# Optimization experiments

Measured on AMD Instinct MI355X. Metric: run time of the kernel, lower is better.

Reference implementation:

```python
import jax, jax.numpy as jnp
import numpy as np

N_NODES = 50000
N_EDGES = 800000
D = 128  # d_feat == hidden_channels


def setup_inputs() -> dict:
    key = jax.random.key(0)
    ks = jax.random.split(key, 7)
    s = 1.0 / np.sqrt(D)
    return {
        "x": jax.random.normal(ks[0], (N_NODES, D), dtype=jnp.float32),
        "edge_index": jax.random.randint(ks[1], (2, N_EDGES), 0, N_NODES, dtype=jnp.int64),
        "W1_l": jax.random.normal(ks[2], (D, D), dtype=jnp.float32) * s,
        "b1": jnp.zeros((D,), dtype=jnp.float32),
        "W1_r": jax.random.normal(ks[3], (D, D), dtype=jnp.float32) * s,
        "W2_l": jax.random.normal(ks[4], (D, D), dtype=jnp.float32) * s,
        "b2": jnp.zeros((D,), dtype=jnp.float32),
        "W2_r": jax.random.normal(ks[5], (D, D), dtype=jnp.float32) * s,
    }


def reference(x, edge_index, W1_l, b1, W1_r, W2_l, b2, W2_r):
    src = edge_index[0]
    dst = edge_index[1]
    n = x.shape[0]
    # in-degree for mean aggregation (zero-degree nodes get 0 aggregate)
    deg = jax.ops.segment_sum(jnp.ones_like(src, dtype=x.dtype), dst, num_segments=n)
    inv_deg = (1.0 / jnp.maximum(deg, 1.0))[:, None]  # [N,1]

    def sage_conv(h, Wl, b, Wr):
        # mean over incoming neighbor messages, then lin_l(agg) + lin_r(h)
        agg = jax.ops.segment_sum(h[src], dst, num_segments=n) * inv_deg  # [N,D]
        return agg @ Wl + b + h @ Wr

    h = jax.nn.relu(sage_conv(x, W1_l, b1, W1_r))
    return sage_conv(h, W2_l, b2, W2_r)
```

## Files before the change

### kernel.cpp

```cpp
#include <hip/hip_runtime.h>
#include <hip/hip_bf16.h>

typedef __attribute__((ext_vector_type(8))) short bf16x8;
typedef __attribute__((ext_vector_type(4))) float f32x4;

#define CAP 64
#define SH  8

static __device__ inline unsigned short f2b(float f) {
    unsigned u = __float_as_uint(f);
    unsigned r = (u + 0x7FFFu + ((u >> 16) & 1u)) >> 16;
    return (unsigned short)r;
}
static __device__ inline float blo(unsigned u) { return __uint_as_float(u << 16); }
static __device__ inline float bhi(unsigned u) { return __uint_as_float(u & 0xFFFF0000u); }

__global__ void zero_kernel(int* __restrict__ p, int n) {
    int i = blockIdx.x * blockDim.x + threadIdx.x;
    if (i < n) p[i] = 0;
}

__global__ __launch_bounds__(256) void fill_shard_kernel(
        const int* __restrict__ ei, int* __restrict__ cursor,
        unsigned short* __restrict__ edge16, int E, int N, int G, int npg) {
    int s = blockIdx.x & (SH - 1);
    int i = blockIdx.x >> 3;
    int d_lo = s * npg;
    int d_hi = d_lo + npg; if (d_hi > N) d_hi = N;
    int C = (E + G - 1) / G;
    int e0 = i * C;
    int e1 = e0 + C; if (e1 > E) e1 = E;
    for (int e = e0 + threadIdx.x; e < e1; e += 256) {
        int d = ei[E + e];
        if (d < d_lo || d >= d_hi) continue;
        int src = ei[e];
        if ((unsigned)src >= (unsigned)N) src = 0;
        int pos = atomicAdd(&cursor[d], 1);
        if (pos < CAP) edge16[(size_t)d * CAP + pos] = (unsigned short)src;
    }
}

__global__ __launch_bounds__(256) void x2b_kernel(const float* __restrict__ x,
                                                  unsigned short* __restrict__ xb,
                                                  int n4) {
    int i = blockIdx.x * blockDim.x + threadIdx.x;
    if (i >= n4) return;
    float4 v = ((const float4*)x)[i];
    ushort4 b;
    b.x = f2b(v.x); b.y = f2b(v.y); b.z = f2b(v.z); b.w = f2b(v.w);
    ((ushort4*)xb)[i] = b;
}

__global__ void prep_w_kernel(const float* __restrict__ W1l, const float* __restrict__ W1r,
                              const float* __restrict__ W2l, const float* __restrict__ W2r,
                              unsigned short* __restrict__ wt) {
    int n = blockIdx.x & 127;
    int layer = blockIdx.x >> 7;
    int k = threadIdx.x;
    const float* Wlp = layer ? W2l : W1l;
    const float* Wrp = layer ? W2r : W1r;
    unsigned short* dst = wt + (size_t)layer * 128 * 256 + (size_t)n * 256;
    dst[k]       = f2b(Wlp[(size_t)k * 128 + n]);
    dst[k + 128] = f2b(Wrp[(size_t)k * 128 + n]);
}

template<int RELU, int OUT_BF16>
__global__ __launch_bounds__(256) void layer_kernel(
        const unsigned short* __restrict__ in, const int* __restrict__ cursor,
        const unsigned short* __restrict__ edge16, const int* __restrict__ ei,
        const unsigned short* __restrict__ Wt, const float* __restrict__ bias,
        void* __restrict__ outp, int E, int N) {
    constexpr int LDK = 264;
    __shared__ unsigned short sA[64 * LDK];
    int tid  = threadIdx.x;
    int lane = tid & 63;
    int wave = tid >> 6;
    int row0 = blockIdx.x * 64;

    #pragma unroll
    for (int it = 0; it < 4; ++it) {
        int c = tid + it * 256;
        int r = c >> 4;
        int q = c & 15;
        int row = row0 + r; if (row >= N) row = N - 1;
        uint4 v = ((const uint4*)(in + (size_t)row * 128))[q];
        *(uint4*)&sA[r * LDK + 128 + q * 8] = v;
    }

    int g = lane >> 4;
    int f = lane & 15;
    for (int i = 0; i < 16; ++i) {
        int node = row0 + wave * 16 + i;
        if (node >= N) break;
        int deg = cursor[node];
        float acc[8];
        #pragma unroll
        for (int t = 0; t < 8; ++t) acc[t] = 0.f;

        if (deg <= CAP) {
            const unsigned short* base = edge16 + (size_t)node * CAP;
            int idx = (lane < deg) ? (int)base[lane] : 0;
            #pragma unroll 4
            for (int j = 0; j < deg; j += 4) {
                int e = j + g;
                int s = __shfl(idx, e & 63);
                if (e < deg) {
                    uint4 v = *(const uint4*)(in + (size_t)s * 128 + f * 8);
                    acc[0] += blo(v.x); acc[1] += bhi(v.x);
                    acc[2] += blo(v.y); acc[3] += bhi(v.y);
                    acc[4] += blo(v.z); acc[5] += bhi(v.z);
                    acc[6] += blo(v.w); acc[7] += bhi(v.w);
                }
            }
        } else {
            for (int j = 0; j < E; j += 4) {
                int e = j + g;
                bool act = (e < E) && (ei[E + e] == node);
                if (act) {
                    int s = ei[e];
                    if ((unsigned)s >= (unsigned)N) s = 0;
                    uint4 v = *(const uint4*)(in + (size_t)s * 128 + f * 8);
                    acc[0] += blo(v.x); acc[1] += bhi(v.x);
                    acc[2] += blo(v.y); acc[3] += bhi(v.y);
                    acc[4] += blo(v.z); acc[5] += bhi(v.z);
                    acc[6] += blo(v.w); acc[7] += bhi(v.w);
                }
            }
        }
        #pragma unroll
        for (int d = 16; d <= 32; d <<= 1) {
            #pragma unroll
            for (int t = 0; t < 8; ++t) acc[t] += __shfl_xor(acc[t], d);
        }
        if (g == 0) {
            float inv = 1.0f / (float)(deg > 1 ? deg : 1);
            uint4 o;
            o.x = (unsigned)f2b(acc[0] * inv) | ((unsigned)f2b(acc[1] * inv) << 16);
            o.y = (unsigned)f2b(acc[2] * inv) | ((unsigned)f2b(acc[3] * inv) << 16);
            o.z = (unsigned)f2b(acc[4] * inv) | ((unsigned)f2b(acc[5] * inv) << 16);
            o.w = (unsigned)f2b(acc[6] * inv) | ((unsigned)f2b(acc[7] * inv) << 16);
            *(uint4*)&sA[(wave * 16 + i) * LDK + f * 8] = o;
        }
    }
    __syncthreads();

    int quad = lane >> 4;
    int tm   = lane & 15;

    f32x4 acc[4][2];
    #pragma unroll
    for (int m = 0; m < 4; ++m)
        #pragma unroll
        for (int j = 0; j < 2; ++j)
            acc[m][j] = (f32x4){0.f, 0.f, 0.f, 0.f};

    const unsigned short* wb0 = Wt + (size_t)(wave * 32 + tm) * 256;

    #pragma unroll
    for (int ks = 0; ks < 8; ++ks) {
        int k0 = ks * 32 + quad * 8;
        bf16x8 a[4], b[2];
        #pragma unroll
        for (int m = 0; m < 4; ++m)
            a[m] = *(const bf16x8*)&sA[(m * 16 + tm) * LDK + k0];
        #pragma unroll
        for (int j = 0; j < 2; ++j)
            b[j] = *(const bf16x8*)(wb0 + (size_t)j * 16 * 256 + k0);
        #pragma unroll
        for (int m = 0; m < 4; ++m)
            #pragma unroll
            for (int j = 0; j < 2; ++j)
                acc[m][j] = __builtin_amdgcn_mfma_f32_16x16x32_bf16(a[m], b[j], acc[m][j], 0, 0, 0);
    }

    #pragma unroll
    for (int j = 0; j < 2; ++j) {
        int ncol = wave * 32 + j * 16 + tm;
        float bb = bias[ncol];
        #pragma unroll
        for (int m = 0; m < 4; ++m) {
            #pragma unroll
            for (int reg = 0; reg < 4; ++reg) {
                int row = row0 + m * 16 + quad * 4 + reg;
                if (row >= N) continue;
                float v = acc[m][j][reg] + bb;
                if (RELU) v = v > 0.f ? v : 0.f;
                if (OUT_BF16)
                    ((unsigned short*)outp)[(size_t)row * 128 + ncol] = f2b(v);
                else
                    ((float*)outp)[(size_t)row * 128 + ncol] = v;
            }
        }
    }
}

extern "C" void kernel_launch(void* const* d_in, const int* in_sizes, int n_in,
                              void* d_out, int out_size, void* d_ws, size_t ws_size,
                              hipStream_t stream) {
    const float* x   = (const float*)d_in[0];
    const int*   ei  = (const int*)d_in[1];
    const float* W1l = (const float*)d_in[2];
    const float* b1  = (const float*)d_in[3];
    const float* W1r = (const float*)d_in[4];
    const float* W2l = (const float*)d_in[5];
    const float* b2  = (const float*)d_in[6];
    const float* W2r = (const float*)d_in[7];
    float* out = (float*)d_out;

    const int D = 128;
    const int N = in_sizes[0] / D;
    const int E = in_sizes[1] / 2;

    char* ws = (char*)d_ws;
    size_t off = 0;
    auto alloc = [&](size_t bytes) {
        size_t o = off;
        off = (off + bytes + 511) & ~(size_t)511;
        return (void*)(ws + o);
    };
    int*            cursor  = (int*)           alloc((size_t)N * 4);
    unsigned short* edge16  = (unsigned short*)alloc((size_t)N * CAP * 2);
    unsigned short* xb      = (unsigned short*)alloc((size_t)N * D * 2);
    unsigned short* h_bf    = (unsigned short*)alloc((size_t)N * D * 2);
    unsigned short* wt      = (unsigned short*)alloc((size_t)2 * 128 * 256 * 2);
    (void)ws_size; (void)n_in; (void)out_size;

    zero_kernel<<<(N + 255) / 256, 256, 0, stream>>>(cursor, N);
    {
        int G = 256;
        int npg = (N + SH - 1) / SH;
        fill_shard_kernel<<<SH * G, 256, 0, stream>>>(ei, cursor, edge16, E, N, G, npg);
    }

    int n4 = N * D / 4;
    x2b_kernel<<<(n4 + 255) / 256, 256, 0, stream>>>(x, xb, n4);
    prep_w_kernel<<<256, 128, 0, stream>>>(W1l, W1r, W2l, W2r, wt);
    const unsigned short* wt1 = wt;
    const unsigned short* wt2 = wt + (size_t)128 * 256;

    int grid = (N + 63) / 64;

    layer_kernel<1, 1><<<grid, 256, 0, stream>>>(xb,   cursor, edge16, ei, wt1, b1, (void*)h_bf, E, N);
    layer_kernel<0, 0><<<grid, 256, 0, stream>>>(h_bf, cursor, edge16, ei, wt2, b2, (void*)out,  E, N);
}
```

Before: 260.4 us.

## Split aggregation into column-chunked gather kernel separate from MFMA GEMM

```diff
diff --git a/kernel.cpp b/kernel.cpp
--- a/kernel.cpp
+++ b/kernel.cpp
@@ -40,57 +40,47 @@
     }
 }
 
-__global__ __launch_bounds__(256) void x2b_kernel(const float* __restrict__ x,
-                                                  unsigned short* __restrict__ xb,
-                                                  int n4) {
-    int i = blockIdx.x * blockDim.x + threadIdx.x;
-    if (i >= n4) return;
-    float4 v = ((const float4*)x)[i];
-    ushort4 b;
-    b.x = f2b(v.x); b.y = f2b(v.y); b.z = f2b(v.z); b.w = f2b(v.w);
-    ((ushort4*)xb)[i] = b;
-}
-
-__global__ void prep_w_kernel(const float* __restrict__ W1l, const float* __restrict__ W1r,
-                              const float* __restrict__ W2l, const float* __restrict__ W2r,
-                              unsigned short* __restrict__ wt) {
-    int n = blockIdx.x & 127;
-    int layer = blockIdx.x >> 7;
-    int k = threadIdx.x;
-    const float* Wlp = layer ? W2l : W1l;
-    const float* Wrp = layer ? W2r : W1r;
-    unsigned short* dst = wt + (size_t)layer * 128 * 256 + (size_t)n * 256;
-    dst[k]       = f2b(Wlp[(size_t)k * 128 + n]);
-    dst[k + 128] = f2b(Wrp[(size_t)k * 128 + n]);
-}
-
-template<int RELU, int OUT_BF16>
-__global__ __launch_bounds__(256) void layer_kernel(
+__global__ __launch_bounds__(256) void convert_kernel(
+        const float* __restrict__ x, unsigned short* __restrict__ xb, int n4,
+        const float* __restrict__ W1l, const float* __restrict__ W1r,
+        const float* __restrict__ W2l, const float* __restrict__ W2r,
+        unsigned short* __restrict__ wt, int G1) {
+    int b = blockIdx.x;
+    if (b < G1) {
+        int i = b * 256 + threadIdx.x;
+        if (i >= n4) return;
+        float4 v = ((const float4*)x)[i];
+        ushort4 o;
+        o.x = f2b(v.x); o.y = f2b(v.y); o.z = f2b(v.z); o.w = f2b(v.w);
+        ((ushort4*)xb)[i] = o;
+    } else {
+        int id = (b - G1) * 256 + threadIdx.x;
+        int layer = id >> 15;
+        int rem = id & 32767;
+        int n = rem >> 8;
+        int kk = rem & 255;
+        const float* Wlp = layer ? W2l : W1l;
+        const float* Wrp = layer ? W2r : W1r;
+        float v = (kk < 128) ? Wlp[(size_t)kk * 128 + n]
+                             : Wrp[(size_t)(kk - 128) * 128 + n];
+        wt[(size_t)layer * 32768 + (size_t)n * 256 + kk] = f2b(v);
+    }
+}
+
+__global__ __launch_bounds__(256) void aggregate_c_kernel(
         const unsigned short* __restrict__ in, const int* __restrict__ cursor,
         const unsigned short* __restrict__ edge16, const int* __restrict__ ei,
-        const unsigned short* __restrict__ Wt, const float* __restrict__ bias,
-        void* __restrict__ outp, int E, int N) {
-    constexpr int LDK = 264;
-    __shared__ unsigned short sA[64 * LDK];
-    int tid  = threadIdx.x;
-    int lane = tid & 63;
-    int wave = tid >> 6;
-    int row0 = blockIdx.x * 64;
-
-    #pragma unroll
-    for (int it = 0; it < 4; ++it) {
-        int c = tid + it * 256;
-        int r = c >> 4;
-        int q = c & 15;
-        int row = row0 + r; if (row >= N) row = N - 1;
-        uint4 v = ((const uint4*)(in + (size_t)row * 128))[q];
-        *(uint4*)&sA[r * LDK + 128 + q * 8] = v;
-    }
-
-    int g = lane >> 4;
-    int f = lane & 15;
-    for (int i = 0; i < 16; ++i) {
-        int node = row0 + wave * 16 + i;
+        unsigned short* __restrict__ aggc, int E, int N) {
+    int c    = blockIdx.x & 7;
+    int nb   = blockIdx.x >> 3;
+    int wave = threadIdx.x >> 6;
+    int lane = threadIdx.x & 63;
+    int es   = lane >> 1;
+    int half = lane & 1;
+    int node0 = nb * 16 + wave * 4;
+
+    for (int i = 0; i < 4; ++i) {
+        int node = node0 + i;
         if (node >= N) break;
         int deg = cursor[node];
         float acc[8];
@@ -100,12 +90,11 @@
         if (deg <= CAP) {
             const unsigned short* base = edge16 + (size_t)node * CAP;
             int idx = (lane < deg) ? (int)base[lane] : 0;
-            #pragma unroll 4
-            for (int j = 0; j < deg; j += 4) {
-                int e = j + g;
+            for (int j = 0; j < deg; j += 32) {
+                int e = j + es;
                 int s = __shfl(idx, e & 63);
                 if (e < deg) {
-                    uint4 v = *(const uint4*)(in + (size_t)s * 128 + f * 8);
+                    uint4 v = *(const uint4*)(in + (size_t)s * 128 + c * 16 + half * 8);
                     acc[0] += blo(v.x); acc[1] += bhi(v.x);
                     acc[2] += blo(v.y); acc[3] += bhi(v.y);
                     acc[4] += blo(v.z); acc[5] += bhi(v.z);
@@ -113,13 +102,13 @@
                 }
             }
         } else {
-            for (int j = 0; j < E; j += 4) {
-                int e = j + g;
+            for (int j = 0; j < E; j += 32) {
+                int e = j + es;
                 bool act = (e < E) && (ei[E + e] == node);
                 if (act) {
                     int s = ei[e];
                     if ((unsigned)s >= (unsigned)N) s = 0;
-                    uint4 v = *(const uint4*)(in + (size_t)s * 128 + f * 8);
+                    uint4 v = *(const uint4*)(in + (size_t)s * 128 + c * 16 + half * 8);
                     acc[0] += blo(v.x); acc[1] += bhi(v.x);
                     acc[2] += blo(v.y); acc[3] += bhi(v.y);
                     acc[4] += blo(v.z); acc[5] += bhi(v.z);
@@ -127,23 +116,58 @@
                 }
             }
         }
-        #pragma unroll
-        for (int d = 16; d <= 32; d <<= 1) {
+
+        #pragma unroll
+        for (int d = 2; d <= 32; d <<= 1) {
             #pragma unroll
             for (int t = 0; t < 8; ++t) acc[t] += __shfl_xor(acc[t], d);
         }
-        if (g == 0) {
+
+        if (es == 0) {
             float inv = 1.0f / (float)(deg > 1 ? deg : 1);
             uint4 o;
             o.x = (unsigned)f2b(acc[0] * inv) | ((unsigned)f2b(acc[1] * inv) << 16);
             o.y = (unsigned)f2b(acc[2] * inv) | ((unsigned)f2b(acc[3] * inv) << 16);
             o.z = (unsigned)f2b(acc[4] * inv) | ((unsigned)f2b(acc[5] * inv) << 16);
             o.w = (unsigned)f2b(acc[6] * inv) | ((unsigned)f2b(acc[7] * inv) << 16);
-            *(uint4*)&sA[(wave * 16 + i) * LDK + f * 8] = o;
-        }
+            *(uint4*)(aggc + ((size_t)c * N + node) * 16 + half * 8) = o;
+        }
+    }
+}
+
+template<int RELU, int OUT_BF16>
+__global__ __launch_bounds__(256) void gemm_mfma_kernel(
+        const unsigned short* __restrict__ aggc, const unsigned short* __restrict__ Xrow,
+        const unsigned short* __restrict__ Wt, const float* __restrict__ bias,
+        void* __restrict__ outp, int N) {
+    constexpr int LDK = 264;
+    __shared__ unsigned short sA[64 * LDK];
+    int tid = threadIdx.x;
+    int row0 = blockIdx.x * 64;
+
+    #pragma unroll
+    for (int it = 0; it < 4; ++it) {
+        int f = tid + it * 256;
+        int c = f >> 7;
+        int rr = (f >> 1) & 63;
+        int h = f & 1;
+        int row = row0 + rr; if (row >= N) row = N - 1;
+        uint4 v = *(const uint4*)(aggc + ((size_t)c * N + row) * 16 + h * 8);
+        *(uint4*)&sA[rr * LDK + c * 16 + h * 8] = v;
+    }
+    #pragma unroll
+    for (int it = 0; it < 4; ++it) {
+        int f = tid + it * 256;
+        int rr = f >> 4;
+        int q = f & 15;
+        int row = row0 + rr; if (row >= N) row = N - 1;
+        uint4 v = ((const uint4*)(Xrow + (size_t)row * 128))[q];
+        *(uint4*)&sA[rr * LDK + 128 + q * 8] = v;
     }
     __syncthreads();
 
+    int lane = tid & 63;
+    int wave = tid >> 6;
     int quad = lane >> 4;
     int tm   = lane & 15;
 
@@ -220,9 +244,10 @@
     };
     int*            cursor  = (int*)           alloc((size_t)N * 4);
     unsigned short* edge16  = (unsigned short*)alloc((size_t)N * CAP * 2);
+    unsigned short* aggc    = (unsigned short*)alloc((size_t)N * D * 2);
     unsigned short* xb      = (unsigned short*)alloc((size_t)N * D * 2);
-    unsigned short* h_bf    = (unsigned short*)alloc((size_t)N * D * 2);
     unsigned short* wt      = (unsigned short*)alloc((size_t)2 * 128 * 256 * 2);
+    unsigned short* h_bf = xb;
     (void)ws_size; (void)n_in; (void)out_size;
 
     zero_kernel<<<(N + 255) / 256, 256, 0, stream>>>(cursor, N);
@@ -233,13 +258,17 @@
     }
 
     int n4 = N * D / 4;
-    x2b_kernel<<<(n4 + 255) / 256, 256, 0, stream>>>(x, xb, n4);
-    prep_w_kernel<<<256, 128, 0, stream>>>(W1l, W1r, W2l, W2r, wt);
+    int G1 = (n4 + 255) / 256;
+    convert_kernel<<<G1 + 256, 256, 0, stream>>>(x, xb, n4, W1l, W1r, W2l, W2r, wt, G1);
     const unsigned short* wt1 = wt;
     const unsigned short* wt2 = wt + (size_t)128 * 256;
 
-    int grid = (N + 63) / 64;
-
-    layer_kernel<1, 1><<<grid, 256, 0, stream>>>(xb,   cursor, edge16, ei, wt1, b1, (void*)h_bf, E, N);
-    layer_kernel<0, 0><<<grid, 256, 0, stream>>>(h_bf, cursor, edge16, ei, wt2, b2, (void*)out,  E, N);
-}
+    int agg_grid  = 8 * ((N + 15) / 16);
+    int gemm_grid = (N + 63) / 64;
+
+    aggregate_c_kernel<<<agg_grid, 256, 0, stream>>>(xb, cursor, edge16, ei, aggc, E, N);
+    gemm_mfma_kernel<1, 1><<<gemm_grid, 256, 0, stream>>>(aggc, xb, wt1, b1, (void*)h_bf, N);
+
+    aggregate_c_kernel<<<agg_grid, 256, 0, stream>>>(h_bf, cursor, edge16, ei, aggc, E, N);
+    gemm_mfma_kernel<0, 0><<<gemm_grid, 256, 0, stream>>>(aggc, h_bf, wt2, b2, (void*)out, N);
+}
```

After: 508.9 us. 1.95x slower.
